# Kernel optimization log

Measured on AMD Instinct MI355X. Metric: run time of the kernel, lower is better.

The kernel has to match this reference:

```python
import jax, jax.numpy as jnp
import numpy as np

B, N, M, DIM = 2, 4096, 512, 1024
H, HD = 16, 64
ROT = 32          # sum(axes_dim) = partial rotary dim on keys
INNER = H * HD    # 1024
EPS = 1e-5


def _layernorm(x, g, b):
    mu = jnp.mean(x, axis=-1, keepdims=True)
    var = jnp.mean(jnp.square(x - mu), axis=-1, keepdims=True)
    return (x - mu) * jax.lax.rsqrt(var + EPS) * g + b


def _apply_rotary(k_rope, cos, sin):
    # k_rope: [b, h, n, ROT]; cos/sin: [n, ROT//2]; rotate consecutive pairs
    b, h, n, d = k_rope.shape
    kr = k_rope.reshape(b, h, n, d // 2, 2)
    x0, x1 = kr[..., 0], kr[..., 1]
    c = cos[None, None, :, :]
    s = sin[None, None, :, :]
    r0 = x0 * c - x1 * s
    r1 = x1 * c + x0 * s
    return jnp.stack([r0, r1], axis=-1).reshape(b, h, n, d)


def setup_inputs() -> dict:
    key = jax.random.key(0)
    ks = jax.random.split(key, 12)
    ang = jax.random.uniform(ks[0], (N, ROT // 2), minval=0.0, maxval=2 * np.pi)
    return {
        "x": jax.random.normal(ks[1], (B, N, DIM), dtype=jnp.float32),
        "latents": jax.random.normal(ks[2], (B, M, DIM), dtype=jnp.float32),
        "cos": jnp.cos(ang),
        "sin": jnp.sin(ang),
        "Wq": jax.random.normal(ks[3], (DIM, INNER), dtype=jnp.float32) * 0.02,
        "Wkv": jax.random.normal(ks[4], (DIM, 2 * INNER), dtype=jnp.float32) * 0.02,
        "Wout": jax.random.normal(ks[5], (INNER, DIM), dtype=jnp.float32) * 0.02,
        "gx": jnp.ones((DIM,), jnp.float32),
        "bx": jnp.zeros((DIM,), jnp.float32),
        "gl": jnp.ones((DIM,), jnp.float32),
        "bl": jnp.zeros((DIM,), jnp.float32),
    }


def reference(x, latents, cos, sin, Wq, Wkv, Wout, gx, bx, gl, bl):
    scale = HD ** -0.5
    xn = _layernorm(x, gx, bx)            # [b, n, d]
    ln = _layernorm(latents, gl, bl)      # [b, m, d]

    q = (ln @ Wq).reshape(B, M, H, HD).transpose(0, 2, 1, 3)      # [b,h,m,hd]
    kv_x = xn @ Wkv                                               # [b,n,2*inner]
    k_x, v_x = jnp.split(kv_x, 2, axis=-1)
    k_x = k_x.reshape(B, N, H, HD).transpose(0, 2, 1, 3)          # [b,h,n,hd]
    v_x = v_x.reshape(B, N, H, HD).transpose(0, 2, 1, 3)
    kv_l = ln @ Wkv
    k_l, v_l = jnp.split(kv_l, 2, axis=-1)
    k_l = k_l.reshape(B, M, H, HD).transpose(0, 2, 1, 3)          # [b,h,m,hd]
    v_l = v_l.reshape(B, M, H, HD).transpose(0, 2, 1, 3)

    # partial rotary applied only to keys from x
    k_rope = _apply_rotary(k_x[..., :ROT], cos, sin)
    k_x = jnp.concatenate([k_rope, k_x[..., ROT:]], axis=-1)

    k = jnp.concatenate([k_x, k_l], axis=2)                       # [b,h,n+m,hd]
    v = jnp.concatenate([v_x, v_l], axis=2)

    sim = jnp.einsum('bhid,bhjd->bhij', q * scale, k)             # [b,h,m,n+m]
    attn = jax.nn.softmax(sim, axis=-1)
    out = jnp.einsum('bhij,bhjd->bhid', attn, v)                  # [b,h,m,hd]
    out = out.transpose(0, 2, 1, 3).reshape(B, M, INNER)
    return out @ Wout                                             # [b,m,dim]
```

## Files before the change

### kernel.cpp

```cpp
#include <hip/hip_runtime.h>
#include <hip/hip_bf16.h>

#define DIMW 1024
#define NB 2
#define NSEQ 4096
#define MLAT 512
#define NH 16
#define HDIM 64
#define SKV 4608
#define LNEPS 1e-5f

typedef __attribute__((ext_vector_type(8))) short bf16x8;
typedef __attribute__((ext_vector_type(4))) float f32x4;

static __device__ __forceinline__ ushort f2bf(float f) {
  __hip_bfloat16 h = __float2bfloat16(f);
  return *reinterpret_cast<ushort*>(&h);
}

#define GLOAD_LDS16(gp, lp)                                                    \
  __builtin_amdgcn_global_load_lds(                                            \
      (const __attribute__((address_space(1))) void*)(gp),                     \
      (__attribute__((address_space(3))) void*)(lp), 16, 0, 0)

__global__ __launch_bounds__(256) void ln_kernel(const float* __restrict__ in,
                                                 const float* __restrict__ g,
                                                 const float* __restrict__ bb,
                                                 ushort* __restrict__ out) {
  const int row = blockIdx.x;
  const int tid = threadIdx.x;
  const float4 x = reinterpret_cast<const float4*>(in + (size_t)row * DIMW)[tid];
  float s  = x.x + x.y + x.z + x.w;
  float ss = x.x * x.x + x.y * x.y + x.z * x.z + x.w * x.w;
#pragma unroll
  for (int off = 1; off < 64; off <<= 1) {
    s  += __shfl_xor(s, off);
    ss += __shfl_xor(ss, off);
  }
  __shared__ float red[8];
  const int wid = tid >> 6;
  if ((tid & 63) == 0) { red[wid] = s; red[4 + wid] = ss; }
  __syncthreads();
  const float S  = red[0] + red[1] + red[2] + red[3];
  const float SS = red[4] + red[5] + red[6] + red[7];
  const float mu  = S * (1.0f / DIMW);
  const float var = SS * (1.0f / DIMW) - mu * mu;
  const float rv  = rsqrtf(var + LNEPS);
  const float4 g4 = reinterpret_cast<const float4*>(g)[tid];
  const float4 b4 = reinterpret_cast<const float4*>(bb)[tid];
  ushort4 o = make_ushort4(f2bf((x.x - mu) * rv * g4.x + b4.x),
                           f2bf((x.y - mu) * rv * g4.y + b4.y),
                           f2bf((x.z - mu) * rv * g4.z + b4.z),
                           f2bf((x.w - mu) * rv * g4.w + b4.w));
  *reinterpret_cast<ushort4*>(out + (size_t)row * DIMW + tid * 4) = o;
}

__global__ __launch_bounds__(256) void tcast_kernel(const float* __restrict__ W,
                                                    ushort* __restrict__ WT,
                                                    int K, int Nn) {
  __shared__ __align__(16) ushort T[64][72];
  const int t = threadIdx.x;
  const int n0 = blockIdx.x * 64, k0 = blockIdx.y * 64;
#pragma unroll
  for (int i = 0; i < 4; ++i) {
    const int kk = (t >> 4) + 16 * i;
    const int nn = (t & 15) * 4;
    const float4 w = *(const float4*)&W[(size_t)(k0 + kk) * Nn + n0 + nn];
    T[nn + 0][kk] = f2bf(w.x);
    T[nn + 1][kk] = f2bf(w.y);
    T[nn + 2][kk] = f2bf(w.z);
    T[nn + 3][kk] = f2bf(w.w);
  }
  __syncthreads();
#pragma unroll
  for (int i = 0; i < 4; ++i) {
    const int nn = (t >> 4) + 16 * i;
    const int kk = (t & 15) * 4;
    *(ushort4*)&WT[(size_t)(n0 + nn) * K + k0 + kk] = *(ushort4*)&T[nn][kk];
  }
}

template <int MODE>
__global__ __launch_bounds__(256, 2) void gemm_bf16(
    const ushort* __restrict__ A, const ushort* __restrict__ B0,
    const ushort* __restrict__ B1,
    void* __restrict__ o0, ushort* __restrict__ o1, ushort* __restrict__ o2,
    const float* __restrict__ cosT, const float* __restrict__ sinT) {
  __shared__ __align__(16) ushort sm[17408];
  ushort* As = sm;
  ushort* Bs = sm + 8192;

  const int t = threadIdx.x;
  const int lane = t & 63;
  const int wid = t >> 6;
  const int wr = wid >> 1, wc = wid & 1;
  const int arow0 = blockIdx.x * 128;
  const int bcol0 = blockIdx.y * 128;

  const ushort* Bg;
  if (MODE == 1)
    Bg = (bcol0 < 1024) ? (B0 + (size_t)bcol0 * DIMW)
                        : (B1 + (size_t)(bcol0 - 1024) * DIMW);
  else
    Bg = B0 + (size_t)bcol0 * DIMW;
  const ushort* Ag = A + (size_t)arow0 * DIMW;

  const int srow_base = wid * 8;
  const int scol = (lane & 7) * 8;

  f32x4 acc[4][4];
#pragma unroll
  for (int fm = 0; fm < 4; ++fm)
#pragma unroll
    for (int fn = 0; fn < 4; ++fn) acc[fm][fn] = (f32x4)(0.0f);

  const int aoff = (wr * 64 + (lane & 15)) * 64 + (lane >> 4) * 8;
  const int boff = 8192 + (wc * 64 + (lane & 15)) * 64 + (lane >> 4) * 8;

  for (int kt = 0; kt < 16; ++kt) {
    __syncthreads();
#pragma unroll
    for (int r = 0; r < 4; ++r) {
      const int off  = r * 2048 + wid * 512 + lane * 8;
      const int row  = r * 32 + srow_base + (lane >> 3);
      const size_t gofs = (size_t)row * DIMW + kt * 64 + scol;
      GLOAD_LDS16(Ag + gofs, As + off);
      GLOAD_LDS16(Bg + gofs, Bs + off);
    }
    __syncthreads();
#pragma unroll
    for (int s = 0; s < 2; ++s) {
      bf16x8 af[4], bfr[4];
#pragma unroll
      for (int f = 0; f < 4; ++f) {
        af[f]  = *(const bf16x8*)(sm + aoff + f * 16 * 64 + s * 32);
        bfr[f] = *(const bf16x8*)(sm + boff + f * 16 * 64 + s * 32);
      }
#pragma unroll
      for (int fm = 0; fm < 4; ++fm)
#pragma unroll
        for (int fn = 0; fn < 4; ++fn)
          acc[fm][fn] = __builtin_amdgcn_mfma_f32_16x16x32_bf16(
              af[fm], bfr[fn], acc[fm][fn], 0, 0, 0);
    }
  }

  const int lr0 = (lane >> 4) * 4;
  const int lc  = lane & 15;

  if (MODE == 0) {
#pragma unroll
    for (int fm = 0; fm < 4; ++fm)
#pragma unroll
      for (int fn = 0; fn < 4; ++fn)
#pragma unroll
        for (int r = 0; r < 4; ++r) {
          const int row = arow0 + wr * 64 + fm * 16 + lr0 + r;
          const int col = bcol0 + wc * 64 + fn * 16 + lc;
          ((float*)o0)[(size_t)row * DIMW + col] = acc[fm][fn][r];
        }
  } else {
    __syncthreads();
    ushort* Es = sm;
#pragma unroll
    for (int fm = 0; fm < 4; ++fm)
#pragma unroll
      for (int fn = 0; fn < 4; ++fn)
#pragma unroll
        for (int r = 0; r < 4; ++r) {
          const int rl = wr * 64 + fm * 16 + lr0 + r;
          const int cl = wc * 64 + fn * 16 + lc;
          const int row = arow0 + rl;
          const int col = bcol0 + cl;
          float v = acc[fm][fn][r];
          const float p = __shfl_xor(v, 1);
          if (MODE == 1) {
            if (col < 1024) v *= 0.125f;
          } else {
            if (col < 1024) {
              const int hd = col & 63;
              if (hd < 32) {
                const int pos = row & 4095;
                const float cs = cosT[pos * 16 + (hd >> 1)];
                const float sn = sinT[pos * 16 + (hd >> 1)];
                v = (hd & 1) ? fmaf(v, cs, p * sn) : fmaf(v, cs, -p * sn);
              }
            }
          }
          Es[rl * 136 + cl] = f2bf(v);
        }
    __syncthreads();
#pragma unroll
    for (int p8 = 0; p8 < 8; ++p8) {
      const int idx = p8 * 256 + t;
      const int rl  = idx >> 4;
      const int c8  = idx & 15;
      const int row = arow0 + rl;
      const int col0 = bcol0 + c8 * 8;
      const int4 val = *(const int4*)(Es + rl * 136 + c8 * 8);
      ushort* dst;
      if (MODE == 1) {
        const int b = row >> 9, m = row & 511;
        if (col0 < 1024) {
          dst = (ushort*)o0 +
                (size_t)((b * NH + (col0 >> 6)) * MLAT + m) * HDIM + (col0 & 63);
        } else if (col0 < 2048) {
          const int c2 = col0 - 1024;
          dst = o1 + (size_t)((b * NH + (c2 >> 6)) * SKV + NSEQ + m) * HDIM + (c2 & 63);
        } else {
          const int c2 = col0 - 2048;
          dst = o2 + (size_t)((b * NH + (c2 >> 6)) * SKV + NSEQ + m) * HDIM + (c2 & 63);
        }
      } else {
        const int b = row >> 12, pos = row & 4095;
        if (col0 < 1024) {
          dst = o1 + (size_t)((b * NH + (col0 >> 6)) * SKV + pos) * HDIM + (col0 & 63);
        } else {
          const int c2 = col0 - 1024;
          dst = o2 + (size_t)((b * NH + (c2 >> 6)) * SKV + pos) * HDIM + (c2 & 63);
        }
      }
      *(int4*)dst = val;
    }
  }
}

__global__ __launch_bounds__(256) void attn_mfma(const ushort* __restrict__ q,
                                                 const ushort* __restrict__ k,
                                                 const ushort* __restrict__ v,
                                                 ushort* __restrict__ ao) {
  __shared__ __align__(16) ushort sm[20480];
  const int t = threadIdx.x;
  const int l = t & 63;
  const int wid = t >> 6;
  const int qt = blockIdx.x, bh = blockIdx.y;
  const size_t kvb = (size_t)bh * SKV * HDIM;

  bf16x8 qf[2];
  {
    const ushort* qa = q + ((size_t)bh * MLAT + qt * 64 + wid * 16 + (l & 15)) * HDIM
                         + 8 * (l >> 4);
    qf[0] = *(const bf16x8*)(qa);
    qf[1] = *(const bf16x8*)(qa + 32);
  }

  ushort* Kb0 = sm;
  ushort* Kb1 = sm + 4096;
  ushort* Vb0 = sm + 8192;
  ushort* Vb1 = sm + 12288;
  ushort* Pw  = sm + 16384 + wid * 1024;

  const int kr  = t >> 2;
  const int kc0 = t & 3;
  const int vr  = t & 63;
  const int vc0 = (t >> 6) * 2;

  f32x4 accO[4];
#pragma unroll
  for (int fd = 0; fd < 4; ++fd) accO[fd] = (f32x4)(0.0f);
  float mrow[4] = {-1e30f, -1e30f, -1e30f, -1e30f};
  float lrow[4] = {0.0f, 0.0f, 0.0f, 0.0f};

  const ushort* kp = k + kvb;
  const ushort* vp = v + kvb;
  int4 kreg[2], vreg[2];
#pragma unroll
  for (int c = 0; c < 2; ++c) {
    kreg[c] = *(const int4*)(kp + kr * 64 + (kc0 + 4 * c) * 8);
    vreg[c] = *(const int4*)(vp + vr * 64 + (vc0 + c) * 8);
  }

  for (int kt = 0; kt < SKV / 64; ++kt) {
    ushort* Kd = (kt & 1) ? Kb1 : Kb0;
    ushort* Vd = (kt & 1) ? Vb1 : Vb0;
#pragma unroll
    for (int c = 0; c < 2; ++c) {
      const int ch = kc0 + 4 * c;
      *(int4*)(Kd + kr * 64 + ((ch ^ (kr & 7)) * 8)) = kreg[c];
      const int vch = vc0 + c;
      const ushort* src = (const ushort*)&vreg[c];
#pragma unroll
      for (int e = 0; e < 8; ++e) {
        const int d = vch * 8 + e;
        Vd[d * 64 + (vr ^ (8 * (d & 7)))] = src[e];
      }
    }
    if (kt < SKV / 64 - 1) {
      const ushort* kp2 = kp + (size_t)(kt + 1) * 64 * 64;
      const ushort* vp2 = vp + (size_t)(kt + 1) * 64 * 64;
#pragma unroll
      for (int c = 0; c < 2; ++c) {
        kreg[c] = *(const int4*)(kp2 + kr * 64 + (kc0 + 4 * c) * 8);
        vreg[c] = *(const int4*)(vp2 + vr * 64 + (vc0 + c) * 8);
      }
    }
    __syncthreads();

    f32x4 sacc[4];
#pragma unroll
    for (int fn = 0; fn < 4; ++fn) sacc[fn] = (f32x4)(0.0f);
#pragma unroll
    for (int ks = 0; ks < 2; ++ks) {
#pragma unroll
      for (int fn = 0; fn < 4; ++fn) {
        const bf16x8 kf = *(const bf16x8*)(
            Kd + (16 * fn + (l & 15)) * 64 + ((8 * (l >> 4) + 32 * ks) ^ (8 * (l & 7))));
        sacc[fn] = __builtin_amdgcn_mfma_f32_16x16x32_bf16(qf[ks], kf, sacc[fn], 0, 0, 0);
      }
    }

    float pvv[4][4];
    float cf[4];
#pragma unroll
    for (int r = 0; r < 4; ++r) {
      float tmax = fmaxf(fmaxf(sacc[0][r], sacc[1][r]), fmaxf(sacc[2][r], sacc[3][r]));
      tmax = fmaxf(tmax, __shfl_xor(tmax, 1));
      tmax = fmaxf(tmax, __shfl_xor(tmax, 2));
      tmax = fmaxf(tmax, __shfl_xor(tmax, 4));
      tmax = fmaxf(tmax, __shfl_xor(tmax, 8));
      const float mn = fmaxf(mrow[r], tmax);
      cf[r] = __expf(mrow[r] - mn);
      mrow[r] = mn;
      float ts = 0.0f;
#pragma unroll
      for (int fn = 0; fn < 4; ++fn) {
        const float e = __expf(sacc[fn][r] - mn);
        pvv[fn][r] = e;
        ts += e;
      }
      ts += __shfl_xor(ts, 1);
      ts += __shfl_xor(ts, 2);
      ts += __shfl_xor(ts, 4);
      ts += __shfl_xor(ts, 8);
      lrow[r] = lrow[r] * cf[r] + ts;
    }
#pragma unroll
    for (int fd = 0; fd < 4; ++fd)
#pragma unroll
      for (int r = 0; r < 4; ++r) accO[fd][r] *= cf[r];

    const int rbase = 4 * (l >> 4);
#pragma unroll
    for (int fn = 0; fn < 4; ++fn)
#pragma unroll
      for (int r = 0; r < 4; ++r) {
        const int row = rbase + r;
        Pw[row * 64 + ((16 * fn + (l & 15)) ^ (8 * (row & 7)))] = f2bf(pvv[fn][r]);
      }

#pragma unroll
    for (int ks = 0; ks < 2; ++ks) {
      const bf16x8 pa = *(const bf16x8*)(
          Pw + (l & 15) * 64 + ((8 * (l >> 4) + 32 * ks) ^ (8 * (l & 7))));
#pragma unroll
      for (int fd = 0; fd < 4; ++fd) {
        const bf16x8 vf = *(const bf16x8*)(
            Vd + (16 * fd + (l & 15)) * 64 + ((8 * (l >> 4) + 32 * ks) ^ (8 * (l & 7))));
        accO[fd] = __builtin_amdgcn_mfma_f32_16x16x32_bf16(pa, vf, accO[fd], 0, 0, 0);
      }
    }
  }

  const int b = bh >> 4, h = bh & 15;
#pragma unroll
  for (int fd = 0; fd < 4; ++fd)
#pragma unroll
    for (int r = 0; r < 4; ++r) {
      const int m = qt * 64 + wid * 16 + 4 * (l >> 4) + r;
      const float val = accO[fd][r] / lrow[r];
      ao[((size_t)b * MLAT + m) * DIMW + h * HDIM + 16 * fd + (l & 15)] = f2bf(val);
    }
}

extern "C" void kernel_launch(void* const* d_in, const int* in_sizes, int n_in,
                              void* d_out, int out_size, void* d_ws, size_t ws_size,
                              hipStream_t stream) {
  const float* x    = (const float*)d_in[0];
  const float* lat  = (const float*)d_in[1];
  const float* cosT = (const float*)d_in[2];
  const float* sinT = (const float*)d_in[3];
  const float* Wq   = (const float*)d_in[4];
  const float* Wkv  = (const float*)d_in[5];
  const float* Wout = (const float*)d_in[6];
  const float* gx   = (const float*)d_in[7];
  const float* bx   = (const float*)d_in[8];
  const float* gl   = (const float*)d_in[9];
  const float* bl   = (const float*)d_in[10];
  float* out = (float*)d_out;

  ushort* xnb   = (ushort*)d_ws;
  ushort* lnb   = xnb   + (size_t)8192 * 1024;
  ushort* WqT   = lnb   + (size_t)1024 * 1024;
  ushort* WkvT  = WqT   + (size_t)1024 * 1024;
  ushort* WoutT = WkvT  + (size_t)2048 * 1024;
  ushort* qwb   = WoutT + (size_t)1024 * 1024;
  ushort* kwb   = qwb   + (size_t)NB * NH * MLAT * HDIM;
  ushort* vwb   = kwb   + (size_t)NB * NH * SKV * HDIM;
  ushort* aob   = vwb   + (size_t)NB * NH * SKV * HDIM;

  ln_kernel<<<dim3(NB * NSEQ), dim3(256), 0, stream>>>(x, gx, bx, xnb);
  ln_kernel<<<dim3(NB * MLAT), dim3(256), 0, stream>>>(lat, gl, bl, lnb);

  tcast_kernel<<<dim3(16, 16), dim3(256), 0, stream>>>(Wq,   WqT,   DIMW, 1024);
  tcast_kernel<<<dim3(32, 16), dim3(256), 0, stream>>>(Wkv,  WkvT,  DIMW, 2048);
  tcast_kernel<<<dim3(16, 16), dim3(256), 0, stream>>>(Wout, WoutT, DIMW, 1024);

  gemm_bf16<1><<<dim3(8, 24), dim3(256), 0, stream>>>(
      lnb, WqT, WkvT, qwb, kwb, vwb, nullptr, nullptr);
  gemm_bf16<2><<<dim3(64, 16), dim3(256), 0, stream>>>(
      xnb, WkvT, nullptr, nullptr, kwb, vwb, cosT, sinT);

  attn_mfma<<<dim3(8, 32), dim3(256), 0, stream>>>(qwb, kwb, vwb, aob);

  gemm_bf16<0><<<dim3(8, 8), dim3(256), 0, stream>>>(
      aob, WoutT, nullptr, out, nullptr, nullptr, nullptr, nullptr);
}
```

Baseline: 332.0 us.

## Split attention KV sequence across blocks and merge partial results

Attention now uses a split-KV (flash-decoding style) scheme. Each of four splits processes a quarter of the key/value tiles and writes unnormalized fp32 partial outputs plus row max and sum. A new combine kernel rescales and merges them into the bf16 output. The original grid had only 256 blocks, too few to fill the GPU's compute units, and this quadruples the block count. The cost is extra global traffic for the partials and one more kernel launch.

After: 303.2 us. 8.7% less time.

```diff
diff --git a/kernel.cpp b/kernel.cpp
--- a/kernel.cpp
+++ b/kernel.cpp
@@ -9,6 +9,8 @@
 #define HDIM 64
 #define SKV 4608
 #define LNEPS 1e-5f
+#define NSPLIT 4
+#define TILES_PER_SPLIT (SKV / 64 / NSPLIT)
 
 typedef __attribute__((ext_vector_type(8))) short bf16x8;
 typedef __attribute__((ext_vector_type(4))) float f32x4;
@@ -225,16 +227,17 @@
   }
 }
 
-__global__ __launch_bounds__(256) void attn_mfma(const ushort* __restrict__ q,
-                                                 const ushort* __restrict__ k,
-                                                 const ushort* __restrict__ v,
-                                                 ushort* __restrict__ ao) {
+__global__ __launch_bounds__(256) void attn_split(const ushort* __restrict__ q,
+                                                  const ushort* __restrict__ k,
+                                                  const ushort* __restrict__ v,
+                                                  float* __restrict__ Opart,
+                                                  float* __restrict__ Ml) {
   __shared__ __align__(16) ushort sm[20480];
   const int t = threadIdx.x;
   const int l = t & 63;
   const int wid = t >> 6;
-  const int qt = blockIdx.x, bh = blockIdx.y;
-  const size_t kvb = (size_t)bh * SKV * HDIM;
+  const int qt = blockIdx.x, bh = blockIdx.y, sp = blockIdx.z;
+  const size_t kvb = (size_t)bh * SKV * HDIM + (size_t)sp * TILES_PER_SPLIT * 64 * HDIM;
 
   bf16x8 qf[2];
   {
@@ -270,7 +273,7 @@
     vreg[c] = *(const int4*)(vp + vr * 64 + (vc0 + c) * 8);
   }
 
-  for (int kt = 0; kt < SKV / 64; ++kt) {
+  for (int kt = 0; kt < TILES_PER_SPLIT; ++kt) {
     ushort* Kd = (kt & 1) ? Kb1 : Kb0;
     ushort* Vd = (kt & 1) ? Vb1 : Vb0;
 #pragma unroll
@@ -285,7 +288,7 @@
         Vd[d * 64 + (vr ^ (8 * (d & 7)))] = src[e];
       }
     }
-    if (kt < SKV / 64 - 1) {
+    if (kt < TILES_PER_SPLIT - 1) {
       const ushort* kp2 = kp + (size_t)(kt + 1) * 64 * 64;
       const ushort* vp2 = vp + (size_t)(kt + 1) * 64 * 64;
 #pragma unroll
@@ -361,15 +364,74 @@
     }
   }
 
+  const int base = (sp * 32 + bh) * 8 + qt;
+  float* Ob = Opart + (size_t)base * 4096;
+#pragma unroll
+  for (int fd = 0; fd < 4; ++fd)
+#pragma unroll
+    for (int r = 0; r < 4; ++r) {
+      const int row = wid * 16 + 4 * (l >> 4) + r;
+      Ob[row * 64 + 16 * fd + (l & 15)] = accO[fd][r];
+    }
+  if ((l & 15) == 0) {
+#pragma unroll
+    for (int r = 0; r < 4; ++r) {
+      const int row = wid * 16 + 4 * (l >> 4) + r;
+      Ml[(size_t)base * 128 + row * 2]     = mrow[r];
+      Ml[(size_t)base * 128 + row * 2 + 1] = lrow[r];
+    }
+  }
+}
+
+__global__ __launch_bounds__(256) void attn_combine(const float* __restrict__ Opart,
+                                                    const float* __restrict__ Ml,
+                                                    ushort* __restrict__ ao) {
+  const int qt = blockIdx.x, bh = blockIdx.y;
+  const int t = threadIdx.x;
+  const int row = t >> 2;
+  const int c0 = (t & 3) * 16;
   const int b = bh >> 4, h = bh & 15;
-#pragma unroll
-  for (int fd = 0; fd < 4; ++fd)
-#pragma unroll
-    for (int r = 0; r < 4; ++r) {
-      const int m = qt * 64 + wid * 16 + 4 * (l >> 4) + r;
-      const float val = accO[fd][r] / lrow[r];
-      ao[((size_t)b * MLAT + m) * DIMW + h * HDIM + 16 * fd + (l & 15)] = f2bf(val);
-    }
+
+  int bases[NSPLIT];
+  float m[NSPLIT], lv[NSPLIT];
+#pragma unroll
+  for (int s = 0; s < NSPLIT; ++s) {
+    bases[s] = (s * 32 + bh) * 8 + qt;
+    m[s]  = Ml[(size_t)bases[s] * 128 + row * 2];
+    lv[s] = Ml[(size_t)bases[s] * 128 + row * 2 + 1];
+  }
+  float mg = fmaxf(fmaxf(m[0], m[1]), fmaxf(m[2], m[3]));
+  float w[NSPLIT];
+  float lg = 0.0f;
+#pragma unroll
+  for (int s = 0; s < NSPLIT; ++s) {
+    w[s] = __expf(m[s] - mg);
+    lg += lv[s] * w[s];
+  }
+  const float inv = 1.0f / lg;
+
+  float acc[16];
+#pragma unroll
+  for (int j = 0; j < 16; ++j) acc[j] = 0.0f;
+#pragma unroll
+  for (int s = 0; s < NSPLIT; ++s) {
+    const float* Ob = Opart + (size_t)bases[s] * 4096 + row * 64 + c0;
+#pragma unroll
+    for (int j4 = 0; j4 < 4; ++j4) {
+      const float4 v = *(const float4*)(Ob + j4 * 4);
+      acc[j4 * 4 + 0] = fmaf(w[s], v.x, acc[j4 * 4 + 0]);
+      acc[j4 * 4 + 1] = fmaf(w[s], v.y, acc[j4 * 4 + 1]);
+      acc[j4 * 4 + 2] = fmaf(w[s], v.z, acc[j4 * 4 + 2]);
+      acc[j4 * 4 + 3] = fmaf(w[s], v.w, acc[j4 * 4 + 3]);
+    }
+  }
+  ushort* dst = ao + ((size_t)(b * MLAT + qt * 64 + row)) * DIMW + h * HDIM + c0;
+#pragma unroll
+  for (int j4 = 0; j4 < 4; ++j4) {
+    *(ushort4*)(dst + j4 * 4) =
+        make_ushort4(f2bf(acc[j4 * 4 + 0] * inv), f2bf(acc[j4 * 4 + 1] * inv),
+                     f2bf(acc[j4 * 4 + 2] * inv), f2bf(acc[j4 * 4 + 3] * inv));
+  }
 }
 
 extern "C" void kernel_launch(void* const* d_in, const int* in_sizes, int n_in,
@@ -397,6 +459,8 @@
   ushort* kwb   = qwb   + (size_t)NB * NH * MLAT * HDIM;
   ushort* vwb   = kwb   + (size_t)NB * NH * SKV * HDIM;
   ushort* aob   = vwb   + (size_t)NB * NH * SKV * HDIM;
+  float*  opart = (float*)(aob + (size_t)1024 * 1024);
+  float*  mlbuf = opart + (size_t)1024 * 4096;
 
   ln_kernel<<<dim3(NB * NSEQ), dim3(256), 0, stream>>>(x, gx, bx, xnb);
   ln_kernel<<<dim3(NB * MLAT), dim3(256), 0, stream>>>(lat, gl, bl, lnb);
@@ -410,7 +474,9 @@
   gemm_bf16<2><<<dim3(64, 16), dim3(256), 0, stream>>>(
       xnb, WkvT, nullptr, nullptr, kwb, vwb, cosT, sinT);
 
-  attn_mfma<<<dim3(8, 32), dim3(256), 0, stream>>>(qwb, kwb, vwb, aob);
+  attn_split<<<dim3(8, 32, NSPLIT), dim3(256), 0, stream>>>(
+      qwb, kwb, vwb, opart, mlbuf);
+  attn_combine<<<dim3(8, 32), dim3(256), 0, stream>>>(opart, mlbuf, aob);
 
   gemm_bf16<0><<<dim3(8, 8), dim3(256), 0, stream>>>(
       aob, WoutT, nullptr, out, nullptr, nullptr, nullptr, nullptr);
```
